# Optimization experiments

Hardware: AMD Instinct MI355X
Metric: run time of the kernel (lower is better)

## Reference

```python
import jax, jax.numpy as jnp
import numpy as np

NB_NODE = 100000
FT = 256
OUT_FT = 256
NB_REL = 4
BATCH = 8192
DEG = 16  # padded neighbors per (node, relation)


def setup_inputs() -> dict:
    key = jax.random.key(0)
    k1, k2, k3, k4 = jax.random.split(key, 4)
    features = jax.random.normal(k1, (NB_NODE, FT), dtype=jnp.float32)
    neighbor_idx = jax.random.randint(k2, (BATCH, NB_REL, DEG), 0, NB_NODE, dtype=jnp.int32)
    # per-relation GCN weight, scaled like xavier
    W = jax.random.normal(k3, (NB_REL, FT, OUT_FT), dtype=jnp.float32) * (1.0 / np.sqrt(FT))
    b = jnp.zeros((NB_REL, OUT_FT), dtype=jnp.float32)
    prelu_a = jnp.full((1,), 0.25, dtype=jnp.float32)  # nn.PReLU() default single param
    node_list = jax.random.randint(k4, (BATCH,), 0, NB_NODE, dtype=jnp.int32)
    return {"features": features, "neighbor_idx": neighbor_idx, "W": W, "b": b,
            "prelu_a": prelu_a, "node_list": node_list, "k": 0}


def _prelu(x, a):
    return jnp.where(x >= 0, x, a * x)


def reference(features, neighbor_idx, W, b, prelu_a, node_list, k):
    # Ragged per-relation neighbor gather + mean (vectorized form of the
    # python double loop): [B, R, D, F] -> mean over D -> [B, R, F]
    v_in = jnp.mean(features[neighbor_idx], axis=2)
    # Per-relation GCN linear + PReLU: [B, R, F] x [R, F, O] -> [B, R, O]
    h = jnp.einsum('brf,rfo->bro', v_in, W) + b[None, :, :]
    h = _prelu(h, prelu_a[0])
    # isAtt=False branch: mean over relations -> [B, O]
    return jnp.mean(h, axis=1)
```

## Files before the change

kernel.cpp:

```cpp
#include <hip/hip_runtime.h>

#define B_TOT 8192
#define FT    256
#define NREL  4
#define DEG   16
#define BM    16

typedef __attribute__((ext_vector_type(8))) short bf16x8;
typedef __attribute__((ext_vector_type(4))) float f32x4;

static __device__ __forceinline__ unsigned short f2bf(float x) {
    union { float f; unsigned int u; } c; c.f = x;
    unsigned int u = c.u;
    u += 0x7fffu + ((u >> 16) & 1u);
    return (unsigned short)(u >> 16);
}
static __device__ __forceinline__ float bf2f(unsigned short h) {
    union { unsigned int u; float f; } c; c.u = ((unsigned int)h) << 16;
    return c.f;
}

__global__ __launch_bounds__(256) void cvt_feat_k(const float* __restrict__ f,
                                                  unsigned short* __restrict__ fb,
                                                  int n4) {
    int i = blockIdx.x * 256 + threadIdx.x;
    if (i < n4) {
        float4 x = ((const float4*)f)[i];
        ushort4 o;
        o.x = f2bf(x.x); o.y = f2bf(x.y); o.z = f2bf(x.z); o.w = f2bf(x.w);
        ((ushort4*)fb)[i] = o;
    }
}

__global__ __launch_bounds__(256) void wtrans_k(const float* __restrict__ W,
                                                unsigned short* __restrict__ Wt) {
    __shared__ float t[64][65];
    int r = blockIdx.z, ft = blockIdx.y, ot = blockIdx.x;
    int c = threadIdx.x & 63, rw = threadIdx.x >> 6;
    const float* src = W + ((size_t)r * 256 + ft * 64) * 256 + ot * 64;
#pragma unroll
    for (int i = 0; i < 16; ++i) {
        int row = i * 4 + rw;
        t[row][c] = src[(size_t)row * 256 + c];
    }
    __syncthreads();
    unsigned short* dst = Wt + ((size_t)r * 256 + ot * 64) * 256 + ft * 64;
#pragma unroll
    for (int i = 0; i < 16; ++i) {
        int row = i * 4 + rw;
        dst[(size_t)row * 256 + c] = f2bf(t[c][row]);
    }
}

template <bool BF16TAB>
__global__ __launch_bounds__(256) void fused_k(const void* __restrict__ ftab_,
                                               const int* __restrict__ nidx,
                                               const unsigned short* __restrict__ Wt,
                                               const float* __restrict__ bias,
                                               const float* __restrict__ prelu,
                                               float* __restrict__ out) {
    __shared__ int shIdx[BM * NREL * DEG];
    __shared__ unsigned short As[BM][FT + 8];
    const int tid  = threadIdx.x;
    const int lane = tid & 63, w = tid >> 6;
    const int blk  = blockIdx.x;
    const int mrow = lane & 15, quad = lane >> 4;
    const float pa = prelu[0];

    ((int4*)shIdx)[tid] = ((const int4*)(nidx + (size_t)blk * BM * NREL * DEG))[tid];
    __syncthreads();

    const int ncol = w * 64 + mrow;
    f32x4 accO[4] = {};

    for (int r = 0; r < NREL; ++r) {
#pragma unroll
        for (int j = 0; j < 4; ++j) {
            const int m = w * 4 + j;
            const int* ip = shIdx + (m * NREL + r) * DEG;
            const int4 i0 = *(const int4*)(ip);
            const int4 i1 = *(const int4*)(ip + 4);
            const int4 i2 = *(const int4*)(ip + 8);
            const int4 i3 = *(const int4*)(ip + 12);
            float s0 = 0.f, s1 = 0.f, s2 = 0.f, s3 = 0.f;
            if constexpr (BF16TAB) {
                const unsigned short* fb = (const unsigned short*)ftab_;
#define ACC(nn) { const ushort4 x = ((const ushort4*)(fb + (size_t)(nn) * FT))[lane]; \
                  s0 += bf2f(x.x); s1 += bf2f(x.y); s2 += bf2f(x.z); s3 += bf2f(x.w); }
                ACC(i0.x) ACC(i0.y) ACC(i0.z) ACC(i0.w)
                ACC(i1.x) ACC(i1.y) ACC(i1.z) ACC(i1.w)
                ACC(i2.x) ACC(i2.y) ACC(i2.z) ACC(i2.w)
                ACC(i3.x) ACC(i3.y) ACC(i3.z) ACC(i3.w)
#undef ACC
            } else {
                const float* ff = (const float*)ftab_;
#define ACC(nn) { const float4 x = ((const float4*)(ff + (size_t)(nn) * FT))[lane]; \
                  s0 += x.x; s1 += x.y; s2 += x.z; s3 += x.w; }
                ACC(i0.x) ACC(i0.y) ACC(i0.z) ACC(i0.w)
                ACC(i1.x) ACC(i1.y) ACC(i1.z) ACC(i1.w)
                ACC(i2.x) ACC(i2.y) ACC(i2.z) ACC(i2.w)
                ACC(i3.x) ACC(i3.y) ACC(i3.z) ACC(i3.w)
#undef ACC
            }
            const float inv = 1.0f / 16.0f;
            ushort4 o;
            o.x = f2bf(s0 * inv); o.y = f2bf(s1 * inv);
            o.z = f2bf(s2 * inv); o.w = f2bf(s3 * inv);
            *(ushort4*)(&As[m][lane * 4]) = o;
        }
        __syncthreads();

        const unsigned short* bp = Wt + ((size_t)(r * 256 + ncol)) * FT;
        float bv[4];
#pragma unroll
        for (int t = 0; t < 4; ++t) bv[t] = bias[r * 256 + ncol + t * 16];

        f32x4 acc[4] = {};
#pragma unroll
        for (int kk = 0; kk < 8; ++kk) {
            const int k0 = kk * 32 + quad * 8;
            const bf16x8 a  = *(const bf16x8*)(&As[mrow][k0]);
            const bf16x8 b0 = *(const bf16x8*)(bp + k0);
            const bf16x8 b1 = *(const bf16x8*)(bp + 16 * FT + k0);
            const bf16x8 b2 = *(const bf16x8*)(bp + 32 * FT + k0);
            const bf16x8 b3 = *(const bf16x8*)(bp + 48 * FT + k0);
            acc[0] = __builtin_amdgcn_mfma_f32_16x16x32_bf16(a, b0, acc[0], 0, 0, 0);
            acc[1] = __builtin_amdgcn_mfma_f32_16x16x32_bf16(a, b1, acc[1], 0, 0, 0);
            acc[2] = __builtin_amdgcn_mfma_f32_16x16x32_bf16(a, b2, acc[2], 0, 0, 0);
            acc[3] = __builtin_amdgcn_mfma_f32_16x16x32_bf16(a, b3, acc[3], 0, 0, 0);
        }
        __syncthreads();

#pragma unroll
        for (int t = 0; t < 4; ++t)
#pragma unroll
            for (int i = 0; i < 4; ++i) {
                float h = acc[t][i] + bv[t];
                h = (h >= 0.f) ? h : pa * h;
                accO[t][i] += h;
            }
    }

    const size_t rbase = (size_t)(blk * BM + quad * 4) * 256;
#pragma unroll
    for (int t = 0; t < 4; ++t)
#pragma unroll
        for (int i = 0; i < 4; ++i)
            out[rbase + (size_t)i * 256 + ncol + t * 16] = accO[t][i] * 0.25f;
}

extern "C" void kernel_launch(void* const* d_in, const int* in_sizes, int n_in,
                              void* d_out, int out_size, void* d_ws, size_t ws_size,
                              hipStream_t stream) {
    const float* feat  = (const float*)d_in[0];
    const int*   nidx  = (const int*)  d_in[1];
    const float* W     = (const float*)d_in[2];
    const float* bias  = (const float*)d_in[3];
    const float* prelu = (const float*)d_in[4];
    float* out = (float*)d_out;

    const size_t feat_elems = (size_t)in_sizes[0];
    const size_t fb_bytes = feat_elems * 2;
    const size_t wt_bytes = (size_t)NREL * 256 * FT * 2;

    if (ws_size >= fb_bytes + wt_bytes) {
        unsigned short* fb = (unsigned short*)d_ws;
        unsigned short* Wt = fb + feat_elems;
        int n4 = (int)(feat_elems / 4);
        cvt_feat_k<<<(n4 + 255) / 256, 256, 0, stream>>>(feat, fb, n4);
        wtrans_k<<<dim3(4, 4, 4), 256, 0, stream>>>(W, Wt);
        fused_k<true><<<B_TOT / BM, 256, 0, stream>>>(fb, nidx, Wt, bias, prelu, out);
    } else {
        unsigned short* Wt = (unsigned short*)d_ws;
        wtrans_k<<<dim3(4, 4, 4), 256, 0, stream>>>(W, Wt);
        fused_k<false><<<B_TOT / BM, 256, 0, stream>>>(feat, nidx, Wt, bias, prelu, out);
    }
}
```

Baseline: 243.7 us.

## Use 16 waves per block: one row per wave gather, one column tile per wave GEMM

```diff
diff --git a/kernel.cpp b/kernel.cpp
--- a/kernel.cpp
+++ b/kernel.cpp
@@ -53,100 +53,95 @@
 }
 
 template <bool BF16TAB>
-__global__ __launch_bounds__(256) void fused_k(const void* __restrict__ ftab_,
-                                               const int* __restrict__ nidx,
-                                               const unsigned short* __restrict__ Wt,
-                                               const float* __restrict__ bias,
-                                               const float* __restrict__ prelu,
-                                               float* __restrict__ out) {
+__global__ __launch_bounds__(1024, 8) void fused_k(const void* __restrict__ ftab_,
+                                                   const int* __restrict__ nidx,
+                                                   const unsigned short* __restrict__ Wt,
+                                                   const float* __restrict__ bias,
+                                                   const float* __restrict__ prelu,
+                                                   float* __restrict__ out) {
     __shared__ int shIdx[BM * NREL * DEG];
-    __shared__ unsigned short As[BM][FT + 8];
+    __shared__ unsigned short As[NREL][BM][FT + 8];
     const int tid  = threadIdx.x;
     const int lane = tid & 63, w = tid >> 6;
     const int blk  = blockIdx.x;
     const int mrow = lane & 15, quad = lane >> 4;
     const float pa = prelu[0];
 
-    ((int4*)shIdx)[tid] = ((const int4*)(nidx + (size_t)blk * BM * NREL * DEG))[tid];
+    shIdx[tid] = nidx[(size_t)blk * (BM * NREL * DEG) + tid];
     __syncthreads();
 
-    const int ncol = w * 64 + mrow;
-    f32x4 accO[4] = {};
-
-    for (int r = 0; r < NREL; ++r) {
+    const float inv = 1.0f / 16.0f;
+    if constexpr (BF16TAB) {
+        const unsigned short* fb = (const unsigned short*)ftab_;
 #pragma unroll
-        for (int j = 0; j < 4; ++j) {
-            const int m = w * 4 + j;
-            const int* ip = shIdx + (m * NREL + r) * DEG;
-            const int4 i0 = *(const int4*)(ip);
-            const int4 i1 = *(const int4*)(ip + 4);
-            const int4 i2 = *(const int4*)(ip + 8);
-            const int4 i3 = *(const int4*)(ip + 12);
+        for (int rr = 0; rr < NREL; ++rr) {
+            const int* ip = shIdx + (w * NREL + rr) * DEG;
+            ushort4 x[DEG];
+#pragma unroll
+            for (int t = 0; t < DEG; ++t)
+                x[t] = ((const ushort4*)(fb + (size_t)ip[t] * FT))[lane];
             float s0 = 0.f, s1 = 0.f, s2 = 0.f, s3 = 0.f;
-            if constexpr (BF16TAB) {
-                const unsigned short* fb = (const unsigned short*)ftab_;
-#define ACC(nn) { const ushort4 x = ((const ushort4*)(fb + (size_t)(nn) * FT))[lane]; \
-                  s0 += bf2f(x.x); s1 += bf2f(x.y); s2 += bf2f(x.z); s3 += bf2f(x.w); }
-                ACC(i0.x) ACC(i0.y) ACC(i0.z) ACC(i0.w)
-                ACC(i1.x) ACC(i1.y) ACC(i1.z) ACC(i1.w)
-                ACC(i2.x) ACC(i2.y) ACC(i2.z) ACC(i2.w)
-                ACC(i3.x) ACC(i3.y) ACC(i3.z) ACC(i3.w)
-#undef ACC
-            } else {
-                const float* ff = (const float*)ftab_;
-#define ACC(nn) { const float4 x = ((const float4*)(ff + (size_t)(nn) * FT))[lane]; \
-                  s0 += x.x; s1 += x.y; s2 += x.z; s3 += x.w; }
-                ACC(i0.x) ACC(i0.y) ACC(i0.z) ACC(i0.w)
-                ACC(i1.x) ACC(i1.y) ACC(i1.z) ACC(i1.w)
-                ACC(i2.x) ACC(i2.y) ACC(i2.z) ACC(i2.w)
-                ACC(i3.x) ACC(i3.y) ACC(i3.z) ACC(i3.w)
-#undef ACC
+#pragma unroll
+            for (int t = 0; t < DEG; ++t) {
+                s0 += bf2f(x[t].x); s1 += bf2f(x[t].y);
+                s2 += bf2f(x[t].z); s3 += bf2f(x[t].w);
             }
-            const float inv = 1.0f / 16.0f;
             ushort4 o;
             o.x = f2bf(s0 * inv); o.y = f2bf(s1 * inv);
             o.z = f2bf(s2 * inv); o.w = f2bf(s3 * inv);
-            *(ushort4*)(&As[m][lane * 4]) = o;
+            *(ushort4*)(&As[rr][w][lane * 4]) = o;
         }
-        __syncthreads();
+    } else {
+        const float* ff = (const float*)ftab_;
+#pragma unroll
+        for (int rr = 0; rr < NREL; ++rr) {
+            const int* ip = shIdx + (w * NREL + rr) * DEG;
+            float s0 = 0.f, s1 = 0.f, s2 = 0.f, s3 = 0.f;
+#pragma unroll
+            for (int h = 0; h < 2; ++h) {
+                float4 x[8];
+#pragma unroll
+                for (int t = 0; t < 8; ++t)
+                    x[t] = ((const float4*)(ff + (size_t)ip[h * 8 + t] * FT))[lane];
+#pragma unroll
+                for (int t = 0; t < 8; ++t) {
+                    s0 += x[t].x; s1 += x[t].y; s2 += x[t].z; s3 += x[t].w;
+                }
+            }
+            ushort4 o;
+            o.x = f2bf(s0 * inv); o.y = f2bf(s1 * inv);
+            o.z = f2bf(s2 * inv); o.w = f2bf(s3 * inv);
+            *(ushort4*)(&As[rr][w][lane * 4]) = o;
+        }
+    }
+    __syncthreads();
 
+    const int ncol = w * 16 + mrow;
+    f32x4 accO = {};
+#pragma unroll
+    for (int r = 0; r < NREL; ++r) {
         const unsigned short* bp = Wt + ((size_t)(r * 256 + ncol)) * FT;
-        float bv[4];
-#pragma unroll
-        for (int t = 0; t < 4; ++t) bv[t] = bias[r * 256 + ncol + t * 16];
-
-        f32x4 acc[4] = {};
+        const float bv = bias[r * 256 + ncol];
+        f32x4 acc = {};
 #pragma unroll
         for (int kk = 0; kk < 8; ++kk) {
             const int k0 = kk * 32 + quad * 8;
-            const bf16x8 a  = *(const bf16x8*)(&As[mrow][k0]);
-            const bf16x8 b0 = *(const bf16x8*)(bp + k0);
-            const bf16x8 b1 = *(const bf16x8*)(bp + 16 * FT + k0);
-            const bf16x8 b2 = *(const bf16x8*)(bp + 32 * FT + k0);
-            const bf16x8 b3 = *(const bf16x8*)(bp + 48 * FT + k0);
-            acc[0] = __builtin_amdgcn_mfma_f32_16x16x32_bf16(a, b0, acc[0], 0, 0, 0);
-            acc[1] = __builtin_amdgcn_mfma_f32_16x16x32_bf16(a, b1, acc[1], 0, 0, 0);
-            acc[2] = __builtin_amdgcn_mfma_f32_16x16x32_bf16(a, b2, acc[2], 0, 0, 0);
-            acc[3] = __builtin_amdgcn_mfma_f32_16x16x32_bf16(a, b3, acc[3], 0, 0, 0);
+            const bf16x8 a = *(const bf16x8*)(&As[r][mrow][k0]);
+            const bf16x8 b = *(const bf16x8*)(bp + k0);
+            acc = __builtin_amdgcn_mfma_f32_16x16x32_bf16(a, b, acc, 0, 0, 0);
         }
-        __syncthreads();
-
 #pragma unroll
-        for (int t = 0; t < 4; ++t)
-#pragma unroll
-            for (int i = 0; i < 4; ++i) {
-                float h = acc[t][i] + bv[t];
-                h = (h >= 0.f) ? h : pa * h;
-                accO[t][i] += h;
-            }
+        for (int i = 0; i < 4; ++i) {
+            float h = acc[i] + bv;
+            h = (h >= 0.f) ? h : pa * h;
+            accO[i] += h;
+        }
     }
 
-    const size_t rbase = (size_t)(blk * BM + quad * 4) * 256;
+    const size_t rbase = (size_t)(blk * BM + quad * 4) * 256 + ncol;
 #pragma unroll
-    for (int t = 0; t < 4; ++t)
-#pragma unroll
-        for (int i = 0; i < 4; ++i)
-            out[rbase + (size_t)i * 256 + ncol + t * 16] = accO[t][i] * 0.25f;
+    for (int i = 0; i < 4; ++i)
+        out[rbase + (size_t)i * 256] = accO[i] * 0.25f;
 }
 
 extern "C" void kernel_launch(void* const* d_in, const int* in_sizes, int n_in,
@@ -169,10 +164,10 @@
         int n4 = (int)(feat_elems / 4);
         cvt_feat_k<<<(n4 + 255) / 256, 256, 0, stream>>>(feat, fb, n4);
         wtrans_k<<<dim3(4, 4, 4), 256, 0, stream>>>(W, Wt);
-        fused_k<true><<<B_TOT / BM, 256, 0, stream>>>(fb, nidx, Wt, bias, prelu, out);
+        fused_k<true><<<B_TOT / BM, 1024, 0, stream>>>(fb, nidx, Wt, bias, prelu, out);
     } else {
         unsigned short* Wt = (unsigned short*)d_ws;
         wtrans_k<<<dim3(4, 4, 4), 256, 0, stream>>>(W, Wt);
-        fused_k<false><<<B_TOT / BM, 256, 0, stream>>>(feat, nidx, Wt, bias, prelu, out);
+        fused_k<false><<<B_TOT / BM, 1024, 0, stream>>>(feat, nidx, Wt, bias, prelu, out);
     }
 }
```

Result: faster. 229.9 us (-5.7%).
